# Kernel optimization log

Measured on AMD Instinct MI355X. Metric: run time of the kernel, lower is better.

## Reference

```python
import jax, jax.numpy as jnp
import numpy as np

HIDDEN = 1024
B, S = 4, 2048

def setup_inputs() -> dict:
    key = jax.random.key(0)
    k1, k2 = jax.random.split(key)
    hidden_states = jax.random.normal(k1, (B, S, HIDDEN), dtype=jnp.float32)
    # torch nn.Linear weight layout: [out_features, in_features]
    W_proj = jax.random.normal(k2, (3 * HIDDEN, HIDDEN), dtype=jnp.float32) * (1.0 / np.sqrt(HIDDEN))
    b_proj = jnp.zeros((3 * HIDDEN,), dtype=jnp.float32)
    return {"hidden_states": hidden_states, "W_proj": W_proj, "b_proj": b_proj}

def reference(hidden_states, W_proj, b_proj):
    h = hidden_states.shape[-1]
    # fused QKV projection: y = x @ W^T + b
    qkv = jnp.einsum('bsh,oh->bso', hidden_states, W_proj) + b_proj
    q, k, v = jnp.split(qkv, 3, axis=-1)  # each [B,S,H]
    scale = 1.0 / jnp.sqrt(jnp.asarray(h, dtype=q.dtype))
    scores = jnp.einsum('bqh,bkh->bqk', q, k) * scale  # [B,S,S]
    attn = jax.nn.softmax(scores, axis=-1)
    out = jnp.einsum('bqk,bkh->bqh', attn, v)
    return out
```

## Files before the change

kernel.cpp:

```cpp
#include <hip/hip_runtime.h>
#include <stdint.h>

#define HIDDEN 1024
#define BATCH  4
#define SEQ    2048
#define TOKENS (BATCH * SEQ)
#define QKVD   (3 * HIDDEN)

typedef unsigned short u16;
typedef __attribute__((ext_vector_type(8))) short   short8;
typedef __attribute__((ext_vector_type(4))) float   floatx4;

__device__ __forceinline__ u16 f32_bf16_rne(float f) {
    unsigned int u = __float_as_uint(f);
    u += 0x7FFFu + ((u >> 16) & 1u);
    return (u16)(u >> 16);
}

__device__ __forceinline__ void gl16(const u16* g, u16* l) {
    __builtin_amdgcn_global_load_lds(
        (const __attribute__((address_space(1))) void*)g,
        (__attribute__((address_space(3))) void*)l, 16, 0, 0);
}

#define SYNC8() do { __builtin_amdgcn_sched_barrier(0); \
    asm volatile("s_waitcnt vmcnt(8)\n\ts_barrier" ::: "memory"); } while (0)

__global__ __launch_bounds__(256) void cvt2_bf16_kernel(
        const float* __restrict__ sa, const float* __restrict__ sb,
        u16* __restrict__ da, u16* __restrict__ db, int n4a, int n4tot) {
    int i = blockIdx.x * 256 + threadIdx.x;
    if (i >= n4tot) return;
    float4 v;
    if (i < n4a) v = ((const float4*)sa)[i];
    else         v = ((const float4*)sb)[i - n4a];
    ushort4 o;
    o.x = f32_bf16_rne(v.x); o.y = f32_bf16_rne(v.y);
    o.z = f32_bf16_rne(v.z); o.w = f32_bf16_rne(v.w);
    if (i < n4a) ((ushort4*)da)[i] = o;
    else         ((ushort4*)db)[i - n4a] = o;
}

template <int EPI>
__global__ __launch_bounds__(512, 2) void gemm_bt(
        const u16* __restrict__ A, const u16* __restrict__ B,
        void* __restrict__ Cv, const float* __restrict__ bias,
        int K, int lda, int ldb, int ldc,
        size_t sA, size_t sB, size_t sC, float scale) {
    __shared__ __align__(16) u16 lds[4][16384];

    const int t    = threadIdx.x;
    const int lane = t & 63;
    const int wid  = t >> 6;
    const int wr   = wid >> 2;
    const int wc   = wid & 3;
    const int bm   = blockIdx.y * 256;
    const int bn   = blockIdx.x * 256;

    const u16* Ab = A + (size_t)blockIdx.z * sA;
    const u16* Bb = B + (size_t)blockIdx.z * sB;

    const int r0 = t >> 2;
    const int sl = (t & 3) ^ ((r0 >> 1) & 3);
    const u16* gA0 = Ab + (size_t)(bm + r0) * lda + sl * 8;
    const u16* gA1 = gA0 + (size_t)128 * lda;
    const u16* gB0 = Bb + (size_t)(bn + r0) * ldb + sl * 8;
    const u16* gB1 = gB0 + (size_t)128 * ldb;

    const int fr = lane & 15;
    const int kc = lane >> 4;
    const int fo = ((kc ^ ((fr >> 1) & 3)) << 4);
    const int abyte = (wr * 128 + fr) * 64 + fo;
    const int bbyte = 16384 + (wc * 64 + fr) * 64 + fo;

    floatx4 acc[8][4];
#pragma unroll
    for (int i = 0; i < 8; i++)
#pragma unroll
        for (int j = 0; j < 4; j++) acc[i][j] = (floatx4){0.f, 0.f, 0.f, 0.f};

#define STAGE_A(p, scol) \
    gl16(gA0 + (scol), &lds[p][wid * 512]); \
    gl16(gA1 + (scol), &lds[p][4096 + wid * 512]);
#define STAGE_B(p, scol) \
    gl16(gB0 + (scol), &lds[p][8192  + wid * 512]); \
    gl16(gB1 + (scol), &lds[p][12288 + wid * 512]);

#define MF4(MI, AV) \
    acc[MI][0] = __builtin_amdgcn_mfma_f32_16x16x32_bf16(AV, b0, acc[MI][0], 0, 0, 0); \
    acc[MI][1] = __builtin_amdgcn_mfma_f32_16x16x32_bf16(AV, b1, acc[MI][1], 0, 0, 0); \
    acc[MI][2] = __builtin_amdgcn_mfma_f32_16x16x32_bf16(AV, b2, acc[MI][2], 0, 0, 0); \
    acc[MI][3] = __builtin_amdgcn_mfma_f32_16x16x32_bf16(AV, b3, acc[MI][3], 0, 0, 0);

#define STEP(q, p, scol) { \
    const char* base = (const char*)&lds[q][0]; \
     \
    STAGE_A(p, scol); \
    short8 b0 = *(const short8*)(base + bbyte); \
    short8 b1 = *(const short8*)(base + bbyte + 1024); \
    short8 b2 = *(const short8*)(base + bbyte + 2048); \
    short8 b3 = *(const short8*)(base + bbyte + 3072); \
    short8 a0 = *(const short8*)(base + abyte); \
    short8 a1 = *(const short8*)(base + abyte + 1024); \
    short8 a2 = *(const short8*)(base + abyte + 2048); \
    short8 a3 = *(const short8*)(base + abyte + 3072); \
    __builtin_amdgcn_s_setprio(1); \
    MF4(0, a0) MF4(1, a1) MF4(2, a2) MF4(3, a3) \
    __builtin_amdgcn_s_setprio(0); \
     \
    STAGE_B(p, scol); \
    a0 = *(const short8*)(base + abyte + 4096); \
    a1 = *(const short8*)(base + abyte + 5120); \
    a2 = *(const short8*)(base + abyte + 6144); \
    a3 = *(const short8*)(base + abyte + 7168); \
    __builtin_amdgcn_s_setprio(1); \
    MF4(4, a0) MF4(5, a1) MF4(6, a2) MF4(7, a3) \
    __builtin_amdgcn_s_setprio(0); \
    SYNC8(); }

    STAGE_A(0, 0)  STAGE_B(0, 0)
    STAGE_A(1, 32) STAGE_B(1, 32)
    STAGE_A(2, 64) STAGE_B(2, 64)
    SYNC8();

    const int nk = K >> 5;
    for (int kt = 0; kt < nk; kt += 4) {
        const int s0 = (kt + 3 < nk ? kt + 3 : nk - 1) << 5;
        const int s1 = (kt + 4 < nk ? kt + 4 : nk - 1) << 5;
        const int s2 = (kt + 5 < nk ? kt + 5 : nk - 1) << 5;
        const int s3 = (kt + 6 < nk ? kt + 6 : nk - 1) << 5;
        STEP(0, 3, s0)
        STEP(1, 0, s1)
        STEP(2, 1, s2)
        STEP(3, 2, s3)
    }
    asm volatile("s_waitcnt vmcnt(0)" ::: "memory");

#undef STEP
#undef MF4
#undef STAGE_A
#undef STAGE_B

    const int crow0 = bm + wr * 128 + kc * 4;
    const int ccol0 = bn + wc * 64 + fr;
    const size_t coff = (size_t)blockIdx.z * sC;

    if (EPI == 0) {
        u16* C = (u16*)Cv;
        float bv[4];
#pragma unroll
        for (int ni = 0; ni < 4; ni++) bv[ni] = bias[ccol0 + ni * 16];
#pragma unroll
        for (int mi = 0; mi < 8; mi++)
#pragma unroll
            for (int ni = 0; ni < 4; ni++)
#pragma unroll
                for (int r = 0; r < 4; r++)
                    C[coff + (size_t)(crow0 + mi * 16 + r) * ldc + (ccol0 + ni * 16)] =
                        f32_bf16_rne(acc[mi][ni][r] + bv[ni]);
    } else {
        float* C = (float*)Cv;
#pragma unroll
        for (int mi = 0; mi < 8; mi++)
#pragma unroll
            for (int ni = 0; ni < 4; ni++)
#pragma unroll
                for (int r = 0; r < 4; r++) {
                    float v = acc[mi][ni][r];
                    if (EPI == 1) v *= scale;
                    C[coff + (size_t)(crow0 + mi * 16 + r) * ldc + (ccol0 + ni * 16)] = v;
                }
    }
}

__global__ __launch_bounds__(256) void softmax_kernel(
        const float* __restrict__ S, u16* __restrict__ P) {
    __shared__ float redm[4];
    __shared__ float reds[4];
    const size_t base = (size_t)blockIdx.x * SEQ;
    const int t = threadIdx.x, lane = t & 63, wid = t >> 6;
    const float4* src = (const float4*)(S + base);
    float4 a = src[t], b = src[t + 256];

    float m = fmaxf(fmaxf(fmaxf(a.x, a.y), fmaxf(a.z, a.w)),
                    fmaxf(fmaxf(b.x, b.y), fmaxf(b.z, b.w)));
#pragma unroll
    for (int off = 32; off; off >>= 1) m = fmaxf(m, __shfl_xor(m, off, 64));
    if (lane == 0) redm[wid] = m;
    __syncthreads();
    m = fmaxf(fmaxf(redm[0], redm[1]), fmaxf(redm[2], redm[3]));

    float e[8];
    e[0] = __expf(a.x - m); e[1] = __expf(a.y - m);
    e[2] = __expf(a.z - m); e[3] = __expf(a.w - m);
    e[4] = __expf(b.x - m); e[5] = __expf(b.y - m);
    e[6] = __expf(b.z - m); e[7] = __expf(b.w - m);
    float s = e[0] + e[1] + e[2] + e[3] + e[4] + e[5] + e[6] + e[7];
#pragma unroll
    for (int off = 32; off; off >>= 1) s += __shfl_xor(s, off, 64);
    if (lane == 0) reds[wid] = s;
    __syncthreads();
    s = reds[0] + reds[1] + reds[2] + reds[3];
    const float r = 1.f / s;

    ushort4* dst = (ushort4*)(P + base);
    ushort4 o0, o1;
    o0.x = f32_bf16_rne(e[0] * r); o0.y = f32_bf16_rne(e[1] * r);
    o0.z = f32_bf16_rne(e[2] * r); o0.w = f32_bf16_rne(e[3] * r);
    o1.x = f32_bf16_rne(e[4] * r); o1.y = f32_bf16_rne(e[5] * r);
    o1.z = f32_bf16_rne(e[6] * r); o1.w = f32_bf16_rne(e[7] * r);
    dst[t] = o0;
    dst[t + 256] = o1;
}

__global__ __launch_bounds__(256) void transposeV_kernel(
        const u16* __restrict__ qkv, u16* __restrict__ Vt) {
    __shared__ u16 tile[64][66];
    const int b = blockIdx.z;
    const int s0 = blockIdx.x * 64, h0 = blockIdx.y * 64;
    const int t = threadIdx.x;
    const int c = t & 63, r4 = t >> 6;
#pragma unroll
    for (int i = 0; i < 16; i++) {
        int sl = i * 4 + r4;
        tile[sl][c] = qkv[(size_t)(b * SEQ + s0 + sl) * QKVD + 2 * HIDDEN + h0 + c];
    }
    __syncthreads();
#pragma unroll
    for (int i = 0; i < 16; i++) {
        int hl = i * 4 + r4;
        Vt[(size_t)(b * HIDDEN + h0 + hl) * SEQ + s0 + c] = tile[c][hl];
    }
}

extern "C" void kernel_launch(void* const* d_in, const int* in_sizes, int n_in,
                              void* d_out, int out_size, void* d_ws, size_t ws_size,
                              hipStream_t stream) {
    const float* x    = (const float*)d_in[0];
    const float* W    = (const float*)d_in[1];
    const float* bias = (const float*)d_in[2];
    float* out = (float*)d_out;

    u16* Xb  = (u16*)d_ws;
    u16* Wb  = Xb + (size_t)TOKENS * HIDDEN;
    u16* qkv = Wb + (size_t)QKVD * HIDDEN;
    float* scores = (float*)(qkv + (size_t)TOKENS * QKVD);
    u16* P  = (u16*)(scores + (size_t)BATCH * SEQ * SEQ);
    u16* Vt = P + (size_t)BATCH * SEQ * SEQ;

    {
        const int n4a = TOKENS * HIDDEN / 4;
        const int n4b = QKVD * HIDDEN / 4;
        const int n4t = n4a + n4b;
        cvt2_bf16_kernel<<<(n4t + 255) / 256, 256, 0, stream>>>(x, W, Xb, Wb, n4a, n4t);
    }

    gemm_bt<0><<<dim3(QKVD / 256, TOKENS / 256, 1), 512, 0, stream>>>(
        Xb, Wb, qkv, bias, HIDDEN, HIDDEN, HIDDEN, QKVD, 0, 0, 0, 1.f);

    gemm_bt<1><<<dim3(SEQ / 256, SEQ / 256, BATCH), 512, 0, stream>>>(
        qkv, qkv + HIDDEN, scores, nullptr, HIDDEN, QKVD, QKVD, SEQ,
        (size_t)SEQ * QKVD, (size_t)SEQ * QKVD, (size_t)SEQ * SEQ, 0.03125f);

    softmax_kernel<<<BATCH * SEQ, 256, 0, stream>>>(scores, P);

    transposeV_kernel<<<dim3(SEQ / 64, HIDDEN / 64, BATCH), 256, 0, stream>>>(qkv, Vt);

    gemm_bt<2><<<dim3(HIDDEN / 256, SEQ / 256, BATCH), 512, 0, stream>>>(
        P, Vt, out, nullptr, SEQ, SEQ, SEQ, HIDDEN,
        (size_t)SEQ * SEQ, (size_t)HIDDEN * SEQ, (size_t)SEQ * HIDDEN, 1.f);
}
```

Baseline: 280.8 us.

## Restructure GEMM main loop into ping-pong double-buffer with templated M tile

Replaces the four-stage 32-wide K pipeline with a two-buffer scheme over 64-wide K steps. Each step is split into four MFMA quarter-blocks, with fragment reads, async global-to-LDS loads and explicit barriers interleaved between them so compute and loads overlap. The GEMM is now templated on the per-wave M size, and the PV GEMM uses 128-row tiles, which doubles its grid size to fill more CUs. The trade-offs are more barriers per K step and a different LDS footprint, and the hand-written vmcnt accounting must stay correct.

```diff
diff --git a/kernel.cpp b/kernel.cpp
--- a/kernel.cpp
+++ b/kernel.cpp
@@ -23,8 +23,11 @@
         (__attribute__((address_space(3))) void*)l, 16, 0, 0);
 }
 
-#define SYNC8() do { __builtin_amdgcn_sched_barrier(0); \
-    asm volatile("s_waitcnt vmcnt(8)\n\ts_barrier" ::: "memory"); } while (0)
+#define PBAR() do { __builtin_amdgcn_sched_barrier(0); \
+    asm volatile("s_barrier" ::: "memory"); } while (0)
+#define LG0() asm volatile("s_waitcnt lgkmcnt(0)" ::: "memory")
+#define VM4() do { __builtin_amdgcn_sched_barrier(0); \
+    asm volatile("s_waitcnt vmcnt(4)" ::: "memory"); } while (0)
 
 __global__ __launch_bounds__(256) void cvt2_bf16_kernel(
         const float* __restrict__ sa, const float* __restrict__ sb,
@@ -41,20 +44,25 @@
     else         ((ushort4*)db)[i - n4a] = o;
 }
 
-template <int EPI>
+template <int EPI, int WM>
 __global__ __launch_bounds__(512, 2) void gemm_bt(
         const u16* __restrict__ A, const u16* __restrict__ B,
         void* __restrict__ Cv, const float* __restrict__ bias,
         int K, int lda, int ldb, int ldc,
         size_t sA, size_t sB, size_t sC, float scale) {
-    __shared__ __align__(16) u16 lds[4][16384];
+    constexpr int BM    = 2 * WM;
+    constexpr int MIH   = WM / 32;
+    constexpr int ASLAB = BM * 64;
+    constexpr int BSLAB = 256 * 64;
+    constexpr int BUFB  = 2 * ASLAB + 2 * BSLAB;
+    __shared__ __align__(16) char lds[2][BUFB];
 
     const int t    = threadIdx.x;
     const int lane = t & 63;
     const int wid  = t >> 6;
     const int wr   = wid >> 2;
     const int wc   = wid & 3;
-    const int bm   = blockIdx.y * 256;
+    const int bm   = blockIdx.y * BM;
     const int bn   = blockIdx.x * 256;
 
     const u16* Ab = A + (size_t)blockIdx.z * sA;
@@ -67,81 +75,89 @@
     const u16* gB0 = Bb + (size_t)(bn + r0) * ldb + sl * 8;
     const u16* gB1 = gB0 + (size_t)128 * ldb;
 
-    const int fr = lane & 15;
-    const int kc = lane >> 4;
-    const int fo = ((kc ^ ((fr >> 1) & 3)) << 4);
-    const int abyte = (wr * 128 + fr) * 64 + fo;
-    const int bbyte = 16384 + (wc * 64 + fr) * 64 + fo;
-
-    floatx4 acc[8][4];
-#pragma unroll
-    for (int i = 0; i < 8; i++)
+    const int fr  = lane & 15;
+    const int kc  = lane >> 4;
+    const int frb = fr * 64 + ((kc ^ ((fr >> 1) & 3)) << 4);
+
+    floatx4 acc[2 * MIH][4];
+#pragma unroll
+    for (int i = 0; i < 2 * MIH; i++)
 #pragma unroll
         for (int j = 0; j < 4; j++) acc[i][j] = (floatx4){0.f, 0.f, 0.f, 0.f};
 
-#define STAGE_A(p, scol) \
-    gl16(gA0 + (scol), &lds[p][wid * 512]); \
-    gl16(gA1 + (scol), &lds[p][4096 + wid * 512]);
-#define STAGE_B(p, scol) \
-    gl16(gB0 + (scol), &lds[p][8192  + wid * 512]); \
-    gl16(gB1 + (scol), &lds[p][12288 + wid * 512]);
-
-#define MF4(MI, AV) \
-    acc[MI][0] = __builtin_amdgcn_mfma_f32_16x16x32_bf16(AV, b0, acc[MI][0], 0, 0, 0); \
-    acc[MI][1] = __builtin_amdgcn_mfma_f32_16x16x32_bf16(AV, b1, acc[MI][1], 0, 0, 0); \
-    acc[MI][2] = __builtin_amdgcn_mfma_f32_16x16x32_bf16(AV, b2, acc[MI][2], 0, 0, 0); \
-    acc[MI][3] = __builtin_amdgcn_mfma_f32_16x16x32_bf16(AV, b3, acc[MI][3], 0, 0, 0);
-
-#define STEP(q, p, scol) { \
-    const char* base = (const char*)&lds[q][0]; \
-     \
-    STAGE_A(p, scol); \
-    short8 b0 = *(const short8*)(base + bbyte); \
-    short8 b1 = *(const short8*)(base + bbyte + 1024); \
-    short8 b2 = *(const short8*)(base + bbyte + 2048); \
-    short8 b3 = *(const short8*)(base + bbyte + 3072); \
-    short8 a0 = *(const short8*)(base + abyte); \
-    short8 a1 = *(const short8*)(base + abyte + 1024); \
-    short8 a2 = *(const short8*)(base + abyte + 2048); \
-    short8 a3 = *(const short8*)(base + abyte + 3072); \
-    __builtin_amdgcn_s_setprio(1); \
-    MF4(0, a0) MF4(1, a1) MF4(2, a2) MF4(3, a3) \
-    __builtin_amdgcn_s_setprio(0); \
-     \
-    STAGE_B(p, scol); \
-    a0 = *(const short8*)(base + abyte + 4096); \
-    a1 = *(const short8*)(base + abyte + 5120); \
-    a2 = *(const short8*)(base + abyte + 6144); \
-    a3 = *(const short8*)(base + abyte + 7168); \
-    __builtin_amdgcn_s_setprio(1); \
-    MF4(4, a0) MF4(5, a1) MF4(6, a2) MF4(7, a3) \
-    __builtin_amdgcn_s_setprio(0); \
-    SYNC8(); }
-
-    STAGE_A(0, 0)  STAGE_B(0, 0)
-    STAGE_A(1, 32) STAGE_B(1, 32)
-    STAGE_A(2, 64) STAGE_B(2, 64)
-    SYNC8();
-
-    const int nk = K >> 5;
-    for (int kt = 0; kt < nk; kt += 4) {
-        const int s0 = (kt + 3 < nk ? kt + 3 : nk - 1) << 5;
-        const int s1 = (kt + 4 < nk ? kt + 4 : nk - 1) << 5;
-        const int s2 = (kt + 5 < nk ? kt + 5 : nk - 1) << 5;
-        const int s3 = (kt + 6 < nk ? kt + 6 : nk - 1) << 5;
-        STEP(0, 3, s0)
-        STEP(1, 0, s1)
-        STEP(2, 1, s2)
-        STEP(3, 2, s3)
+    short8 aF[MIH][2], bLo[2][2], bHi[2][2];
+
+    auto rdA = [&](short8 (&dst)[MIH][2], const char* bp, int miBase) {
+#pragma unroll
+        for (int m = 0; m < MIH; m++)
+#pragma unroll
+            for (int ks = 0; ks < 2; ks++)
+                dst[m][ks] = *(const short8*)(bp + ks * ASLAB +
+                    (wr * WM + (miBase + m) * 16) * 64 + frb);
+    };
+    auto rdB = [&](short8 (&dst)[2][2], const char* bp, int niBase) {
+#pragma unroll
+        for (int n = 0; n < 2; n++)
+#pragma unroll
+            for (int ks = 0; ks < 2; ks++)
+                dst[n][ks] = *(const short8*)(bp + 2 * ASLAB + ks * BSLAB +
+                    (wc * 64 + (niBase + n) * 16) * 64 + frb);
+    };
+    auto mf = [&](short8 (&av)[MIH][2], short8 (&bv)[2][2], int miB, int niB) {
+        __builtin_amdgcn_s_setprio(1);
+#pragma unroll
+        for (int m = 0; m < MIH; m++)
+#pragma unroll
+            for (int n = 0; n < 2; n++)
+#pragma unroll
+                for (int ks = 0; ks < 2; ks++)
+                    acc[miB + m][niB + n] = __builtin_amdgcn_mfma_f32_16x16x32_bf16(
+                        av[m][ks], bv[n][ks], acc[miB + m][niB + n], 0, 0, 0);
+        __builtin_amdgcn_s_setprio(0);
+    };
+
+#define STA(buf, ks, sc) do { \
+    char* d = &lds[buf][(ks) * ASLAB] + wid * 1024; \
+    gl16(gA0 + (sc) + (ks) * 32, (u16*)d); \
+    if constexpr (WM == 128) gl16(gA1 + (sc) + (ks) * 32, (u16*)(d + 8192)); \
+  } while (0)
+#define STB(buf, ks, sc) do { \
+    char* d = &lds[buf][2 * ASLAB + (ks) * BSLAB] + wid * 1024; \
+    gl16(gB0 + (sc) + (ks) * 32, (u16*)d); \
+    gl16(gB1 + (sc) + (ks) * 32, (u16*)(d + 8192)); \
+  } while (0)
+
+#define GROUP(q, S1, S2, S3, S4) { \
+    const char* bp = &lds[q][0]; \
+    rdA(aF, bp, 0); rdB(bLo, bp, 0); S1; PBAR(); LG0(); \
+    mf(aF, bLo, 0, 0);   PBAR(); \
+    rdB(bHi, bp, 2);                S2; PBAR(); LG0(); \
+    mf(aF, bHi, 0, 2);   PBAR(); \
+    rdA(aF, bp, MIH);               S3; PBAR(); LG0(); \
+    mf(aF, bHi, MIH, 2); PBAR(); \
+    S4; VM4(); PBAR(); \
+    mf(aF, bLo, MIH, 0); PBAR(); \
+}
+
+    STA(0, 0, 0); STA(0, 1, 0); STB(0, 0, 0); STB(0, 1, 0);
+    STB(1, 0, 64); STB(1, 1, 64);
+    VM4(); PBAR();
+
+    const int nk = K >> 6;
+    for (int T = 0; T < nk; T += 2) {
+        const int c1 = (T + 1) << 6;
+        const int c2 = (T + 2 < nk ? T + 2 : nk - 1) << 6;
+        const int c3 = (T + 3 < nk ? T + 3 : nk - 1) << 6;
+        GROUP(0, STA(1, 0, c1), STA(1, 1, c1), STB(0, 0, c2), STB(0, 1, c2))
+        GROUP(1, STA(0, 0, c2), STA(0, 1, c2), STB(1, 0, c3), STB(1, 1, c3))
     }
     asm volatile("s_waitcnt vmcnt(0)" ::: "memory");
 
-#undef STEP
-#undef MF4
-#undef STAGE_A
-#undef STAGE_B
-
-    const int crow0 = bm + wr * 128 + kc * 4;
+#undef GROUP
+#undef STB
+#undef STA
+
+    const int crow0 = bm + wr * WM + kc * 4;
     const int ccol0 = bn + wc * 64 + fr;
     const size_t coff = (size_t)blockIdx.z * sC;
 
@@ -151,7 +167,7 @@
 #pragma unroll
         for (int ni = 0; ni < 4; ni++) bv[ni] = bias[ccol0 + ni * 16];
 #pragma unroll
-        for (int mi = 0; mi < 8; mi++)
+        for (int mi = 0; mi < 2 * MIH; mi++)
 #pragma unroll
             for (int ni = 0; ni < 4; ni++)
 #pragma unroll
@@ -161,7 +177,7 @@
     } else {
         float* C = (float*)Cv;
 #pragma unroll
-        for (int mi = 0; mi < 8; mi++)
+        for (int mi = 0; mi < 2 * MIH; mi++)
 #pragma unroll
             for (int ni = 0; ni < 4; ni++)
 #pragma unroll
@@ -255,10 +271,10 @@
         cvt2_bf16_kernel<<<(n4t + 255) / 256, 256, 0, stream>>>(x, W, Xb, Wb, n4a, n4t);
     }
 
-    gemm_bt<0><<<dim3(QKVD / 256, TOKENS / 256, 1), 512, 0, stream>>>(
+    gemm_bt<0, 128><<<dim3(QKVD / 256, TOKENS / 256, 1), 512, 0, stream>>>(
         Xb, Wb, qkv, bias, HIDDEN, HIDDEN, HIDDEN, QKVD, 0, 0, 0, 1.f);
 
-    gemm_bt<1><<<dim3(SEQ / 256, SEQ / 256, BATCH), 512, 0, stream>>>(
+    gemm_bt<1, 128><<<dim3(SEQ / 256, SEQ / 256, BATCH), 512, 0, stream>>>(
         qkv, qkv + HIDDEN, scores, nullptr, HIDDEN, QKVD, QKVD, SEQ,
         (size_t)SEQ * QKVD, (size_t)SEQ * QKVD, (size_t)SEQ * SEQ, 0.03125f);
 
@@ -266,7 +282,7 @@
 
     transposeV_kernel<<<dim3(SEQ / 64, HIDDEN / 64, BATCH), 256, 0, stream>>>(qkv, Vt);
 
-    gemm_bt<2><<<dim3(HIDDEN / 256, SEQ / 256, BATCH), 512, 0, stream>>>(
+    gemm_bt<2, 64><<<dim3(HIDDEN / 256, SEQ / 128, BATCH), 512, 0, stream>>>(
         P, Vt, out, nullptr, SEQ, SEQ, SEQ, HIDDEN,
         (size_t)SEQ * SEQ, (size_t)HIDDEN * SEQ, (size_t)SEQ * HIDDEN, 1.f);
 }
```

Measured after the change: 258.2 us. -8.1%, faster.
